# Kernel optimization log

Hardware: AMD Instinct MI355X
Metric: run time of the kernel (lower is better)

Reference implementation:

```python
import jax, jax.numpy as jnp
import numpy as np

N = 50000
E = 800000
D = 128
L = 3
EPS = 1e-5


def setup_inputs() -> dict:
    key = jax.random.key(0)
    ks = jax.random.split(key, 8)
    x = jax.random.normal(ks[0], (N, D), dtype=jnp.float32)
    edge_index = jax.random.randint(ks[1], (2, E), 0, N, dtype=jnp.int64)
    s = 1.0 / np.sqrt(D)
    # stacked per-layer params (all layers are 128->128)
    Wl = jax.random.uniform(ks[2], (L, D, D), jnp.float32, -s, s)  # lin_l weight
    bl = jax.random.uniform(ks[3], (L, D), jnp.float32, -s, s)     # lin_l bias
    Wr = jax.random.uniform(ks[4], (L, D, D), jnp.float32, -s, s)  # lin_r weight (no bias)
    gamma = jnp.ones((L, D), jnp.float32)
    beta = jnp.zeros((L, D), jnp.float32)
    return {"x": x, "edge_index": edge_index, "Wl": Wl, "bl": bl,
            "Wr": Wr, "gamma": gamma, "beta": beta}


def layer_norm(h, g, b):
    mu = jnp.mean(h, axis=-1, keepdims=True)
    var = jnp.mean(jnp.square(h - mu), axis=-1, keepdims=True)
    return (h - mu) * jax.lax.rsqrt(var + EPS) * g + b


def reference(x, edge_index, Wl, bl, Wr, gamma, beta):
    src = edge_index[0]
    dst = edge_index[1]
    # in-degree counts (constant wrt features)
    cnt = jax.ops.segment_sum(jnp.ones((E,), jnp.float32), dst, num_segments=N)
    inv_cnt = (1.0 / jnp.maximum(cnt, 1.0))[:, None]  # [N,1]
    h = x
    for l in range(L):
        # mean neighbor aggregation: gather source feats, scatter-add to dst
        agg = jax.ops.segment_sum(h[src], dst, num_segments=N) * inv_cnt
        # SAGEConv: lin_l(agg) + lin_r(h)
        h2 = agg @ Wl[l].T + bl[l] + h @ Wr[l].T
        h2 = layer_norm(h2, gamma[l], beta[l])
        h = jax.nn.relu(h2)  # dropout is identity at inference
    return h
```

## Files before the change

kernel.cpp:

```cpp
#include <hip/hip_runtime.h>
#include <hip/hip_bf16.h>
#include <stdint.h>

#define NN 50000
#define EE 800000
#define DD 128
#define LL 3
#define FILL_CHUNKS 196
#define FILL_PER 4096

typedef __attribute__((ext_vector_type(8))) short short8;
typedef __attribute__((ext_vector_type(4))) float float4v;

__device__ __forceinline__ float bf2f(unsigned int u) {
  union { unsigned int i; float f; } x; x.i = u << 16; return x.f;
}
__device__ __forceinline__ unsigned short f2bf(float f) {
  union { float f; unsigned int i; } x; x.f = f;
  unsigned int r = x.i + 0x7FFFu + ((x.i >> 16) & 1u);
  return (unsigned short)(r >> 16);
}

__global__ void deg_kernel(const int* __restrict__ dst, int* __restrict__ deg, int E) {
  int t = blockIdx.x * blockDim.x + threadIdx.x;
  int e = t * 4;
  if (e + 3 < E) {
    int4 d = *(const int4*)(dst + e);
    atomicAdd(&deg[d.x], 1);
    atomicAdd(&deg[d.y], 1);
    atomicAdd(&deg[d.z], 1);
    atomicAdd(&deg[d.w], 1);
  } else {
    for (int i = e; i < E; i++) atomicAdd(&deg[dst[i]], 1);
  }
}

__global__ __launch_bounds__(256) void scan1_kernel(
    const int* __restrict__ deg, int* __restrict__ incl, int* __restrict__ partial, int N) {
  __shared__ int wsums[4];
  const int tid = threadIdx.x, lane = tid & 63, wid = tid >> 6;
  int i = blockIdx.x * 256 + tid;
  int v = (i < N) ? deg[i] : 0;
  int x = v;
#pragma unroll
  for (int off = 1; off < 64; off <<= 1) {
    int y = __shfl_up(x, off, 64);
    if (lane >= off) x += y;
  }
  if (lane == 63) wsums[wid] = x;
  __syncthreads();
  if (tid == 0) {
    int a0 = wsums[0], a1 = wsums[1], a2 = wsums[2];
    wsums[0] = 0; wsums[1] = a0; wsums[2] = a0 + a1; wsums[3] = a0 + a1 + a2;
  }
  __syncthreads();
  int inc = wsums[wid] + x;
  if (i < N) incl[i] = inc;
  if (tid == 255) partial[blockIdx.x] = inc;
}

__global__ __launch_bounds__(256) void scan2_kernel(int* __restrict__ partial, int P) {
  __shared__ int wsums[4];
  const int tid = threadIdx.x, lane = tid & 63, wid = tid >> 6;
  int v = (tid < P) ? partial[tid] : 0;
  int x = v;
#pragma unroll
  for (int off = 1; off < 64; off <<= 1) {
    int y = __shfl_up(x, off, 64);
    if (lane >= off) x += y;
  }
  if (lane == 63) wsums[wid] = x;
  __syncthreads();
  if (tid == 0) {
    int a0 = wsums[0], a1 = wsums[1], a2 = wsums[2];
    wsums[0] = 0; wsums[1] = a0; wsums[2] = a0 + a1; wsums[3] = a0 + a1 + a2;
  }
  __syncthreads();
  int excl = wsums[wid] + x - v;
  if (tid < P) partial[tid] = excl;
}

__global__ __launch_bounds__(256) void scan3_kernel(
    const int* __restrict__ incl, const int* __restrict__ deg, const int* __restrict__ partial,
    int* __restrict__ rowptr, int* __restrict__ cursor, int N) {
  int i = blockIdx.x * 256 + threadIdx.x;
  if (i < N) {
    int rp = incl[i] - deg[i] + partial[blockIdx.x];
    rowptr[i] = rp;
    cursor[i] = rp;
  }
  if (i == 0) rowptr[N] = EE;
}

__global__ __launch_bounds__(256) void fill_kernel(
    const int* __restrict__ src, const int* __restrict__ dst,
    int* __restrict__ cursor, int* __restrict__ col, int E) {
  const int range = blockIdx.x & 7;
  const int chunk = blockIdx.x >> 3;
  const int lo = range * (NN / 8);
  const int hi = lo + (NN / 8);
  const int e0 = chunk * FILL_PER;
  const int e1 = (e0 + FILL_PER < E) ? (e0 + FILL_PER) : E;
  for (int eb = e0 + threadIdx.x * 8; eb < e1; eb += 256 * 8) {
    if (eb + 7 < e1) {
      int4 d4a = *(const int4*)(dst + eb);
      int4 d4b = *(const int4*)(dst + eb + 4);
      int dd[8] = {d4a.x, d4a.y, d4a.z, d4a.w, d4b.x, d4b.y, d4b.z, d4b.w};
      bool m[8];
      int sv[8], pos[8];
#pragma unroll
      for (int j = 0; j < 8; j++) m[j] = (dd[j] >= lo) & (dd[j] < hi);
#pragma unroll
      for (int j = 0; j < 8; j++) if (m[j]) sv[j] = src[eb + j];
#pragma unroll
      for (int j = 0; j < 8; j++) if (m[j]) pos[j] = atomicAdd(&cursor[dd[j]], 1);
#pragma unroll
      for (int j = 0; j < 8; j++) if (m[j]) col[pos[j]] = sv[j];
    } else {
      for (int e = eb; e < e1; e++) {
        int d = dst[e];
        if (d >= lo && d < hi) {
          int pos = atomicAdd(&cursor[d], 1);
          col[pos] = src[e];
        }
      }
    }
  }
}

__global__ void convert_kernel(const float* __restrict__ x, unsigned short* __restrict__ hbf, int n4) {
  int i = blockIdx.x * blockDim.x + threadIdx.x;
  if (i < n4) {
    float4 v = ((const float4*)x)[i];
    ushort4 o;
    o.x = f2bf(v.x); o.y = f2bf(v.y); o.z = f2bf(v.z); o.w = f2bf(v.w);
    ((ushort4*)hbf)[i] = o;
  }
}

__global__ void repack_kernel(const float* __restrict__ Wl, const float* __restrict__ Wr,
                              unsigned short* __restrict__ out) {
  int tid = blockIdx.x * blockDim.x + threadIdx.x;
  if (tid >= LL * 8 * 8 * 64) return;
  int lane = tid & 63;
  int t = (tid >> 6) & 7;
  int ks = (tid >> 9) & 7;
  int l = tid >> 12;
  int n = t * 16 + (lane & 15);
  int kbase = ks * 32 + (lane >> 4) * 8;
  const float* Wsrc = (ks < 4) ? (Wl + ((size_t)(l * 128 + n) * 128 + kbase))
                               : (Wr + ((size_t)(l * 128 + n) * 128 + (kbase - 128)));
#pragma unroll
  for (int j = 0; j < 8; j++) out[(size_t)tid * 8 + j] = f2bf(Wsrc[j]);
}

__global__ __launch_bounds__(256) void agg_kernel(
    const unsigned short* __restrict__ hbf, const int* __restrict__ rowptr,
    const int* __restrict__ col, unsigned short* __restrict__ agg, int N) {
  int node = blockIdx.x * 4 + (threadIdx.x >> 6);
  if (node >= N) return;
  int lane = threadIdx.x & 63;
  const int half = lane >> 5;
  const int l32 = lane & 31;
  int s = rowptr[node], e = rowptr[node + 1];
  float a0 = 0.f, a1 = 0.f, a2 = 0.f, a3 = 0.f;
  int i = s;
  for (; i + 15 < e; i += 16) {
    int idx[8];
#pragma unroll
    for (int j = 0; j < 8; j++) idx[j] = col[i + 2 * j + half];
    uint2 r[8];
#pragma unroll
    for (int j = 0; j < 8; j++) r[j] = ((const uint2*)(hbf + (size_t)idx[j] * 128))[l32];
#pragma unroll
    for (int j = 0; j < 8; j++) {
      a0 += bf2f(r[j].x & 0xffffu); a1 += bf2f(r[j].x >> 16);
      a2 += bf2f(r[j].y & 0xffffu); a3 += bf2f(r[j].y >> 16);
    }
  }
  if (i + 7 < e) {
    int idx[4];
#pragma unroll
    for (int j = 0; j < 4; j++) idx[j] = col[i + 2 * j + half];
    uint2 r[4];
#pragma unroll
    for (int j = 0; j < 4; j++) r[j] = ((const uint2*)(hbf + (size_t)idx[j] * 128))[l32];
#pragma unroll
    for (int j = 0; j < 4; j++) {
      a0 += bf2f(r[j].x & 0xffffu); a1 += bf2f(r[j].x >> 16);
      a2 += bf2f(r[j].y & 0xffffu); a3 += bf2f(r[j].y >> 16);
    }
    i += 8;
  }
  if (i + 3 < e) {
    int idx[2];
#pragma unroll
    for (int j = 0; j < 2; j++) idx[j] = col[i + 2 * j + half];
    uint2 r[2];
#pragma unroll
    for (int j = 0; j < 2; j++) r[j] = ((const uint2*)(hbf + (size_t)idx[j] * 128))[l32];
#pragma unroll
    for (int j = 0; j < 2; j++) {
      a0 += bf2f(r[j].x & 0xffffu); a1 += bf2f(r[j].x >> 16);
      a2 += bf2f(r[j].y & 0xffffu); a3 += bf2f(r[j].y >> 16);
    }
    i += 4;
  }
  if (i + 1 < e) {
    int idx = col[i + half];
    uint2 r = ((const uint2*)(hbf + (size_t)idx * 128))[l32];
    a0 += bf2f(r.x & 0xffffu); a1 += bf2f(r.x >> 16);
    a2 += bf2f(r.y & 0xffffu); a3 += bf2f(r.y >> 16);
    i += 2;
  }
  if (i < e && half == 0) {
    int idx = col[i];
    uint2 r = ((const uint2*)(hbf + (size_t)idx * 128))[l32];
    a0 += bf2f(r.x & 0xffffu); a1 += bf2f(r.x >> 16);
    a2 += bf2f(r.y & 0xffffu); a3 += bf2f(r.y >> 16);
  }
  a0 += __shfl_xor(a0, 32);
  a1 += __shfl_xor(a1, 32);
  a2 += __shfl_xor(a2, 32);
  a3 += __shfl_xor(a3, 32);
  int dg = e - s;
  float inv = 1.0f / (float)(dg > 1 ? dg : 1);
  if (half == 0) {
    uint2 o;
    o.x = ((unsigned int)f2bf(a1 * inv) << 16) | (unsigned int)f2bf(a0 * inv);
    o.y = ((unsigned int)f2bf(a3 * inv) << 16) | (unsigned int)f2bf(a2 * inv);
    ((uint2*)(agg + (size_t)node * 128))[l32] = o;
  }
}

template <bool LAST>
__global__ __launch_bounds__(256) void gemm_ln_mfma_kernel(
    const unsigned short* __restrict__ agg, const unsigned short* __restrict__ h,
    const unsigned short* __restrict__ Bf, const float* __restrict__ bias,
    const float* __restrict__ gamma, const float* __restrict__ beta,
    unsigned short* __restrict__ out_bf, float* __restrict__ f_out, int N) {
  __shared__ unsigned short Bl[8 * 8 * 512];
  __shared__ float reds[64][16];
  __shared__ float redss[64][16];
  __shared__ float mu_s[64], rs_s[64];
  const int tid = threadIdx.x;
  {
    const uint4* srcB = (const uint4*)Bf;
    uint4* dstB = (uint4*)Bl;
#pragma unroll
    for (int i = 0; i < 16; i++) dstB[tid + i * 256] = srcB[tid + i * 256];
  }
  __syncthreads();
  const int wave = tid >> 6, lane = tid & 63;
  const int ln16 = lane & 15, quad = lane >> 4;
  const int m0 = blockIdx.x * 64 + wave * 16;
  int row_a = m0 + ln16;
  if (row_a > N - 1) row_a = N - 1;
  const size_t aoff = (size_t)row_a * 128 + quad * 8;

  float4v acc[8];
#pragma unroll
  for (int t = 0; t < 8; t++) acc[t] = (float4v)0.f;

#pragma unroll
  for (int ks = 0; ks < 8; ks++) {
    const unsigned short* ap = (ks < 4) ? (agg + aoff + ks * 32) : (h + aoff + (ks - 4) * 32);
    short8 a = *(const short8*)ap;
#pragma unroll
    for (int t = 0; t < 8; t++) {
      short8 b = *(const short8*)&Bl[(ks * 8 + t) * 512 + lane * 8];
      acc[t] = __builtin_amdgcn_mfma_f32_16x16x32_bf16(a, b, acc[t], 0, 0, 0);
    }
  }

  float bias_v[8], g_v[8], b_v[8];
#pragma unroll
  for (int t = 0; t < 8; t++) {
    int c = t * 16 + ln16;
    bias_v[t] = bias[c]; g_v[t] = gamma[c]; b_v[t] = beta[c];
  }
#pragma unroll
  for (int r = 0; r < 4; r++) {
    float s = 0.f, ss = 0.f;
#pragma unroll
    for (int t = 0; t < 8; t++) {
      float val = acc[t][r] + bias_v[t];
      s += val; ss += val * val;
    }
    int rowblk = wave * 16 + quad * 4 + r;
    reds[rowblk][ln16] = s;
    redss[rowblk][ln16] = ss;
  }
  __syncthreads();
  if (tid < 64) {
    float s = 0.f, ss = 0.f;
#pragma unroll
    for (int g = 0; g < 16; g++) { s += reds[tid][g]; ss += redss[tid][g]; }
    float mu = s * (1.0f / 128.0f);
    float var = ss * (1.0f / 128.0f) - mu * mu;
    if (var < 0.f) var = 0.f;
    mu_s[tid] = mu;
    rs_s[tid] = rsqrtf(var + 1e-5f);
  }
  __syncthreads();
#pragma unroll
  for (int r = 0; r < 4; r++) {
    int row = m0 + quad * 4 + r;
    int rowblk = wave * 16 + quad * 4 + r;
    if (row < N) {
      float mu = mu_s[rowblk], rs = rs_s[rowblk];
#pragma unroll
      for (int t = 0; t < 8; t++) {
        float val = acc[t][r] + bias_v[t];
        float y = (val - mu) * rs * g_v[t] + b_v[t];
        y = y > 0.f ? y : 0.f;
        int cidx = t * 16 + ln16;
        if (LAST) {
          f_out[(size_t)row * 128 + cidx] = y;
        } else {
          out_bf[(size_t)row * 128 + cidx] = f2bf(y);
        }
      }
    }
  }
}

extern "C" void kernel_launch(void* const* d_in, const int* in_sizes, int n_in,
                              void* d_out, int out_size, void* d_ws, size_t ws_size,
                              hipStream_t stream) {
  const float* x = (const float*)d_in[0];
  const int* edge = (const int*)d_in[1];
  const float* Wl = (const float*)d_in[2];
  const float* bl = (const float*)d_in[3];
  const float* Wr = (const float*)d_in[4];
  const float* gamma = (const float*)d_in[5];
  const float* beta = (const float*)d_in[6];
  float* out = (float*)d_out;

  const int* srcv = edge;
  const int* dstv = edge + EE;

  char* p = (char*)d_ws;
  auto alloc = [&](size_t bytes) {
    char* r = p;
    p += (bytes + 255) & ~(size_t)255;
    return r;
  };
  const size_t bplane = (size_t)NN * 128 * 2;
  unsigned short* xB = (unsigned short*)alloc(bplane);
  unsigned short* h1B = (unsigned short*)alloc(bplane);
  unsigned short* h2B = (unsigned short*)alloc(bplane);
  unsigned short* agB = (unsigned short*)alloc(bplane);
  unsigned short* BfB = (unsigned short*)alloc((size_t)LL * 32768 * 2);
  int* deg = (int*)alloc((size_t)NN * 4);
  int* incl = (int*)alloc((size_t)NN * 4);
  int* cursor = (int*)alloc((size_t)NN * 4);
  int* rowptr = (int*)alloc((size_t)(NN + 1) * 4);
  int* colarr = (int*)alloc((size_t)EE * 4);
  int* partial = (int*)alloc((size_t)256 * 4);
  if ((size_t)(p - (char*)d_ws) > ws_size) return;

  const int SCAN_BLOCKS = (NN + 255) / 256;

  hipMemsetAsync(deg, 0, (size_t)NN * 4, stream);
  deg_kernel<<<(EE / 4 + 255) / 256, 256, 0, stream>>>(dstv, deg, EE);
  scan1_kernel<<<SCAN_BLOCKS, 256, 0, stream>>>(deg, incl, partial, NN);
  scan2_kernel<<<1, 256, 0, stream>>>(partial, SCAN_BLOCKS);
  scan3_kernel<<<SCAN_BLOCKS, 256, 0, stream>>>(incl, deg, partial, rowptr, cursor, NN);
  fill_kernel<<<8 * FILL_CHUNKS, 256, 0, stream>>>(srcv, dstv, cursor, colarr, EE);
  convert_kernel<<<(NN * 128 / 4 + 255) / 256, 256, 0, stream>>>(x, xB, NN * 128 / 4);
  repack_kernel<<<(LL * 4096 + 255) / 256, 256, 0, stream>>>(Wl, Wr, BfB);

  const int gemm_grid = (NN + 63) / 64;
  const int agg_grid = (NN + 3) / 4;

  agg_kernel<<<agg_grid, 256, 0, stream>>>(xB, rowptr, colarr, agB, NN);
  gemm_ln_mfma_kernel<false><<<gemm_grid, 256, 0, stream>>>(
      agB, xB, BfB, bl, gamma, beta, h1B, nullptr, NN);

  agg_kernel<<<agg_grid, 256, 0, stream>>>(h1B, rowptr, colarr, agB, NN);
  gemm_ln_mfma_kernel<false><<<gemm_grid, 256, 0, stream>>>(
      agB, h1B, BfB + 32768, bl + 128, gamma + 128, beta + 128, h2B, nullptr, NN);

  agg_kernel<<<agg_grid, 256, 0, stream>>>(h2B, rowptr, colarr, agB, NN);
  gemm_ln_mfma_kernel<true><<<gemm_grid, 256, 0, stream>>>(
      agB, h2B, BfB + 2 * 32768, bl + 256, gamma + 256, beta + 256, nullptr, out, NN);
}
```

Before: 309.7 us.

## Bucket edges by destination range before CSR fill to avoid rereading all edges

Fuses degree counting with a partition pass that splits the edges into 8 destination-range buckets, staging them in LDS and appending them to global segments. The fill kernel then reads only its own bucket instead of having each of the 8 range blocks scan the whole edge list. This cuts redundant edge reads in the fill step but adds a bucket write and read plus a fixed per-bucket capacity. If a bucket ever exceeds that capacity, edges are silently dropped.

```diff
diff --git a/kernel.cpp b/kernel.cpp
--- a/kernel.cpp
+++ b/kernel.cpp
@@ -6,8 +6,10 @@
 #define EE 800000
 #define DD 128
 #define LL 3
-#define FILL_CHUNKS 196
-#define FILL_PER 4096
+#define NRANGE 8
+#define RSPAN (NN / NRANGE)
+#define CAPA 256
+#define CAPSEG 104000
 
 typedef __attribute__((ext_vector_type(8))) short short8;
 typedef __attribute__((ext_vector_type(4))) float float4v;
@@ -21,17 +23,72 @@
   return (unsigned short)(r >> 16);
 }
 
-__global__ void deg_kernel(const int* __restrict__ dst, int* __restrict__ deg, int E) {
-  int t = blockIdx.x * blockDim.x + threadIdx.x;
-  int e = t * 4;
-  if (e + 3 < E) {
-    int4 d = *(const int4*)(dst + e);
-    atomicAdd(&deg[d.x], 1);
-    atomicAdd(&deg[d.y], 1);
-    atomicAdd(&deg[d.z], 1);
-    atomicAdd(&deg[d.w], 1);
+__global__ __launch_bounds__(256) void bucket_kernel(
+    const int* __restrict__ src, const int* __restrict__ dst,
+    int* __restrict__ deg, int* __restrict__ bcur, uint2* __restrict__ bkt, int E) {
+  __shared__ int cnt[NRANGE];
+  __shared__ int gbase[NRANGE];
+  __shared__ uint2 stage[NRANGE][CAPA];
+  const int tid = threadIdx.x;
+  const int lane = tid & 63;
+  if (tid < NRANGE) cnt[tid] = 0;
+  __syncthreads();
+
+  const int e0 = blockIdx.x * 1024 + tid * 4;
+  int dv[4], sv[4];
+  bool valid[4];
+#pragma unroll
+  for (int j = 0; j < 4; j++) valid[j] = (e0 + j) < E;
+  if (e0 + 3 < E) {
+    int4 d4 = *(const int4*)(dst + e0);
+    int4 s4 = *(const int4*)(src + e0);
+    dv[0] = d4.x; dv[1] = d4.y; dv[2] = d4.z; dv[3] = d4.w;
+    sv[0] = s4.x; sv[1] = s4.y; sv[2] = s4.z; sv[3] = s4.w;
   } else {
-    for (int i = e; i < E; i++) atomicAdd(&deg[dst[i]], 1);
+#pragma unroll
+    for (int j = 0; j < 4; j++) {
+      dv[j] = valid[j] ? dst[e0 + j] : 0;
+      sv[j] = valid[j] ? src[e0 + j] : 0;
+    }
+  }
+#pragma unroll
+  for (int j = 0; j < 4; j++) if (valid[j]) atomicAdd(&deg[dv[j]], 1);
+
+  const unsigned long long ltmask = (1ull << lane) - 1ull;
+#pragma unroll
+  for (int j = 0; j < 4; j++) {
+    int r = valid[j] ? (dv[j] / RSPAN) : -1;
+#pragma unroll
+    for (int rr = 0; rr < NRANGE; rr++) {
+      unsigned long long mask = __ballot(r == rr);
+      if (mask == 0ull) continue;
+      int leader = __ffsll((long long)mask) - 1;
+      int base = 0;
+      if (lane == leader) base = atomicAdd(&cnt[rr], (int)__popcll(mask));
+      base = __shfl(base, leader, 64);
+      if (r == rr) {
+        int pos = base + (int)__popcll(mask & ltmask);
+        uint2 pr; pr.x = (unsigned)sv[j]; pr.y = (unsigned)dv[j];
+        if (pos < CAPA) {
+          stage[rr][pos] = pr;
+        } else {
+          int gpos = atomicAdd(&bcur[rr], 1);
+          if (gpos < CAPSEG) bkt[(size_t)rr * CAPSEG + gpos] = pr;
+        }
+      }
+    }
+  }
+  __syncthreads();
+  if (tid < NRANGE) {
+    int c = cnt[tid]; if (c > CAPA) c = CAPA;
+    cnt[tid] = c;
+    gbase[tid] = atomicAdd(&bcur[tid], c);
+  }
+  __syncthreads();
+#pragma unroll
+  for (int r = 0; r < NRANGE; r++) {
+    int c = cnt[r], gb = gbase[r];
+    for (int k = tid; k < c; k += 256) bkt[(size_t)r * CAPSEG + gb + k] = stage[r][k];
   }
 }
 
@@ -92,37 +149,31 @@
   if (i == 0) rowptr[N] = EE;
 }
 
-__global__ __launch_bounds__(256) void fill_kernel(
-    const int* __restrict__ src, const int* __restrict__ dst,
-    int* __restrict__ cursor, int* __restrict__ col, int E) {
-  const int range = blockIdx.x & 7;
+__global__ __launch_bounds__(256) void fill2_kernel(
+    const int* __restrict__ bcur, const uint2* __restrict__ bkt,
+    int* __restrict__ cursor, int* __restrict__ col) {
+  const int r = blockIdx.x & 7;
   const int chunk = blockIdx.x >> 3;
-  const int lo = range * (NN / 8);
-  const int hi = lo + (NN / 8);
-  const int e0 = chunk * FILL_PER;
-  const int e1 = (e0 + FILL_PER < E) ? (e0 + FILL_PER) : E;
-  for (int eb = e0 + threadIdx.x * 8; eb < e1; eb += 256 * 8) {
-    if (eb + 7 < e1) {
-      int4 d4a = *(const int4*)(dst + eb);
-      int4 d4b = *(const int4*)(dst + eb + 4);
-      int dd[8] = {d4a.x, d4a.y, d4a.z, d4a.w, d4b.x, d4b.y, d4b.z, d4b.w};
-      bool m[8];
-      int sv[8], pos[8];
-#pragma unroll
-      for (int j = 0; j < 8; j++) m[j] = (dd[j] >= lo) & (dd[j] < hi);
-#pragma unroll
-      for (int j = 0; j < 8; j++) if (m[j]) sv[j] = src[eb + j];
-#pragma unroll
-      for (int j = 0; j < 8; j++) if (m[j]) pos[j] = atomicAdd(&cursor[dd[j]], 1);
-#pragma unroll
-      for (int j = 0; j < 8; j++) if (m[j]) col[pos[j]] = sv[j];
+  const int nchunk = (int)(gridDim.x >> 3);
+  int cnt = bcur[r];
+  if (cnt > CAPSEG) cnt = CAPSEG;
+  const int per = (cnt + nchunk - 1) / nchunk;
+  const int i0 = chunk * per;
+  int i1 = i0 + per; if (i1 > cnt) i1 = cnt;
+  const uint2* seg = bkt + (size_t)r * CAPSEG;
+  for (int ib = i0 + threadIdx.x * 4; ib < i1; ib += 256 * 4) {
+    if (ib + 3 < i1) {
+      uint2 p0 = seg[ib], p1 = seg[ib + 1], p2 = seg[ib + 2], p3 = seg[ib + 3];
+      int q0 = atomicAdd(&cursor[p0.y], 1);
+      int q1 = atomicAdd(&cursor[p1.y], 1);
+      int q2 = atomicAdd(&cursor[p2.y], 1);
+      int q3 = atomicAdd(&cursor[p3.y], 1);
+      col[q0] = p0.x; col[q1] = p1.x; col[q2] = p2.x; col[q3] = p3.x;
     } else {
-      for (int e = eb; e < e1; e++) {
-        int d = dst[e];
-        if (d >= lo && d < hi) {
-          int pos = atomicAdd(&cursor[d], 1);
-          col[pos] = src[e];
-        }
+      for (int i = ib; i < i1; i++) {
+        uint2 p = seg[i];
+        int q = atomicAdd(&cursor[p.y], 1);
+        col[q] = p.x;
       }
     }
   }
@@ -352,22 +403,25 @@
   unsigned short* h2B = (unsigned short*)alloc(bplane);
   unsigned short* agB = (unsigned short*)alloc(bplane);
   unsigned short* BfB = (unsigned short*)alloc((size_t)LL * 32768 * 2);
-  int* deg = (int*)alloc((size_t)NN * 4);
+  int* degzone = (int*)alloc((size_t)(NN + 64) * 4);
+  int* deg = degzone;
+  int* bcur = degzone + NN;
   int* incl = (int*)alloc((size_t)NN * 4);
   int* cursor = (int*)alloc((size_t)NN * 4);
   int* rowptr = (int*)alloc((size_t)(NN + 1) * 4);
   int* colarr = (int*)alloc((size_t)EE * 4);
   int* partial = (int*)alloc((size_t)256 * 4);
+  uint2* bkt = (uint2*)alloc((size_t)NRANGE * CAPSEG * 8);
   if ((size_t)(p - (char*)d_ws) > ws_size) return;
 
   const int SCAN_BLOCKS = (NN + 255) / 256;
 
-  hipMemsetAsync(deg, 0, (size_t)NN * 4, stream);
-  deg_kernel<<<(EE / 4 + 255) / 256, 256, 0, stream>>>(dstv, deg, EE);
+  hipMemsetAsync(degzone, 0, (size_t)(NN + 64) * 4, stream);
+  bucket_kernel<<<(EE + 1023) / 1024, 256, 0, stream>>>(srcv, dstv, deg, bcur, bkt, EE);
   scan1_kernel<<<SCAN_BLOCKS, 256, 0, stream>>>(deg, incl, partial, NN);
   scan2_kernel<<<1, 256, 0, stream>>>(partial, SCAN_BLOCKS);
   scan3_kernel<<<SCAN_BLOCKS, 256, 0, stream>>>(incl, deg, partial, rowptr, cursor, NN);
-  fill_kernel<<<8 * FILL_CHUNKS, 256, 0, stream>>>(srcv, dstv, cursor, colarr, EE);
+  fill2_kernel<<<8 * 98, 256, 0, stream>>>(bcur, bkt, cursor, colarr);
   convert_kernel<<<(NN * 128 / 4 + 255) / 256, 256, 0, stream>>>(x, xB, NN * 128 / 4);
   repack_kernel<<<(LL * 4096 + 255) / 256, 256, 0, stream>>>(Wl, Wr, BfB);
 
```

Result: no change. 315.0 us (+1.7%).
